# Optimization experiments

Measured on AMD Instinct MI355X. Metric: run time of the kernel, lower is better.

Reference implementation:

```python
import jax, jax.numpy as jnp
import numpy as np

B, S, DMAX, NMEL, DM, K = 8, 100, 12, 80, 128, 9
T = S * DMAX  # 1200 max mel frames
EPS = 1e-5  # BatchNorm eps (eval mode, running_mean=0, running_var=1)


def setup_inputs() -> dict:
    key = jax.random.key(0)
    ks = jax.random.split(key, 16)
    durations = jax.random.randint(ks[0], (B, S), 4, DMAX + 1).astype(jnp.int32)
    mel_len = jnp.sum(durations, axis=1).astype(jnp.int32)
    src_len = jnp.full((B,), S, dtype=jnp.int32)
    mel = jax.random.normal(ks[1], (B, T, NMEL), dtype=jnp.float32)
    # conv stack params (xavier-ish uniform)
    s1 = float(np.sqrt(6.0 / (1 * K + DM * K)))
    w1 = jax.random.uniform(ks[2], (DM, 1, 1, K), minval=-s1, maxval=s1, dtype=jnp.float32)
    g1 = 1.0 + 0.1 * jax.random.normal(ks[3], (DM,), dtype=jnp.float32)
    be1 = 0.1 * jax.random.normal(ks[4], (DM,), dtype=jnp.float32)
    s2 = float(np.sqrt(6.0 / (DM * K + 1 * K)))
    w2 = jax.random.uniform(ks[5], (1, DM, 1, K), minval=-s2, maxval=s2, dtype=jnp.float32)
    g2 = 1.0 + 0.1 * jax.random.normal(ks[6], (1,), dtype=jnp.float32)
    be2 = 0.1 * jax.random.normal(ks[7], (1,), dtype=jnp.float32)
    # BiGRU params (pytorch layout: gates [r|z|n] stacked -> 3*H rows)
    sh = float(1.0 / np.sqrt(DM))
    u = lambda k, shape: jax.random.uniform(k, shape, minval=-sh, maxval=sh, dtype=jnp.float32)
    w_ih_f = u(ks[8], (3 * DM, NMEL)); w_hh_f = u(ks[9], (3 * DM, DM))
    b_ih_f = u(ks[10], (3 * DM,));    b_hh_f = u(ks[11], (3 * DM,))
    w_ih_b = u(ks[12], (3 * DM, NMEL)); w_hh_b = u(ks[13], (3 * DM, DM))
    b_ih_b = u(ks[14], (3 * DM,));    b_hh_b = u(ks[15], (3 * DM,))
    return {"mel": mel, "durations": durations, "mel_len": mel_len, "src_len": src_len,
            "w1": w1, "g1": g1, "be1": be1, "w2": w2, "g2": g2, "be2": be2,
            "w_ih_f": w_ih_f, "w_hh_f": w_hh_f, "b_ih_f": b_ih_f, "b_hh_f": b_hh_f,
            "w_ih_b": w_ih_b, "w_hh_b": w_hh_b, "b_ih_b": b_ih_b, "b_hh_b": b_hh_b}


def _bn_eval(x, g, b):
    # eval-mode BatchNorm2d with running_mean=0, running_var=1; x [B,C,T,M]
    scale = g / jnp.sqrt(1.0 + EPS)
    return x * scale[None, :, None, None] + b[None, :, None, None]


def _gru_scan(xs_seq, reset_seq, w_hh, b_hh):
    # xs_seq [T,B,3H] precomputed input projections; reset_seq [T,B] 1.0 -> reset h to 0
    H = w_hh.shape[1]
    Bn = xs_seq.shape[1]

    def step(h, inp):
        xg, rst = inp
        h = h * (1.0 - rst)[:, None]
        hg = h @ w_hh.T + b_hh
        xr, xz, xn = jnp.split(xg, 3, axis=-1)
        hr, hz, hn = jnp.split(hg, 3, axis=-1)
        r = jax.nn.sigmoid(xr + hr)
        z = jax.nn.sigmoid(xz + hz)
        n = jnp.tanh(xn + r * hn)
        h_new = (1.0 - z) * n + z * h
        return h_new, h_new

    h0 = jnp.zeros((Bn, H), xs_seq.dtype)
    _, hs = jax.lax.scan(step, h0, (xs_seq, reset_seq))
    return hs  # [T,B,H]


def reference(mel, durations, mel_len, src_len, w1, g1, be1, w2, g2, be2,
              w_ih_f, w_hh_f, b_ih_f, b_hh_f, w_ih_b, w_hh_b, b_ih_b, b_hh_b):
    pad = (K - 1) // 2
    # conv stack: kernel (1,K) mixes only the mel-channel axis -> apply to full mel once
    x = mel[:, None, :, :]  # [B,1,T,M]
    x = jax.lax.conv_general_dilated(x, w1, (1, 1), [(0, 0), (pad, pad)])
    x = jax.nn.relu(_bn_eval(x, g1, be1))
    x = jax.lax.conv_general_dilated(x, w2, (1, 1), [(0, 0), (pad, pad)])
    x = jax.nn.relu(_bn_eval(x, g2, be2))
    x = x[:, 0]  # [B,T,M]

    # segment boundaries from durations (all phones valid here, durations > 0)
    cum = jnp.cumsum(durations, axis=1)      # [B,S]
    starts = cum - durations                 # segment start frame per phone
    ends = cum - 1                           # segment end frame per phone
    bidx = jnp.arange(B)[:, None]
    start_mask = jnp.zeros((B, T), x.dtype).at[bidx, starts].set(1.0)
    end_mask = jnp.zeros((B, T), x.dtype).at[bidx, ends].set(1.0)

    # forward direction: reset h at segment starts, read h at segment ends
    xf = jnp.einsum('btm,gm->tbg', x, w_ih_f) + b_ih_f
    Hf = _gru_scan(xf, start_mask.T, w_hh_f, b_hh_f)           # [T,B,H]
    # backward direction: scan reversed time, reset at original segment ends
    xb = jnp.einsum('btm,gm->tbg', x, w_ih_b) + b_ih_b
    Hb = _gru_scan(xb[::-1], end_mask.T[::-1], w_hh_b, b_hh_b)[::-1]  # [T,B,H], orig time

    hf = jnp.take_along_axis(jnp.transpose(Hf, (1, 0, 2)), ends[..., None], axis=1)    # [B,S,H]
    hb = jnp.take_along_axis(jnp.transpose(Hb, (1, 0, 2)), starts[..., None], axis=1)  # [B,S,H]
    out = jnp.concatenate([hf, hb], axis=-1)  # [B,S,2H]
    valid = (jnp.arange(S)[None, :] < src_len[:, None])[..., None]
    return jnp.where(valid, out, 0.0)
```

## Files before the change

### kernel.cpp

```cpp
#include <hip/hip_runtime.h>
#include <math.h>

#define BB   8
#define SS   100
#define TT   1200
#define NM   80
#define DMC  128
#define KK   9
#define G3   384
#define NROW (BB*TT)

typedef __attribute__((ext_vector_type(8))) short short8;
typedef __attribute__((ext_vector_type(4))) float f32x4;
typedef __attribute__((ext_vector_type(2))) float f32x2;

__device__ __forceinline__ float sigmoid_(float v) { return 1.f / (1.f + __expf(-v)); }
__device__ __forceinline__ float tanh_(float v) {
    float a = fabsf(v);
    float e = __expf(-2.f * a);
    float t = (1.f - e) / (1.f + e);
    return copysignf(t, v);
}
__device__ __forceinline__ unsigned short f2bf(float f) {
    unsigned int u = __float_as_uint(f);
    unsigned int r = (u + 0x7fffu + ((u >> 16) & 1u)) >> 16;
    return (unsigned short)r;
}
__device__ __forceinline__ f32x2 pk_fma(f32x2 a, f32x2 b, f32x2 c) {
    f32x2 d;
    asm("v_pk_fma_f32 %0, %1, %2, %3" : "=v"(d) : "v"(a), "v"(b), "v"(c));
    return d;
}
__device__ __forceinline__ f32x2 pk_add(f32x2 a, f32x2 b) {
    f32x2 d;
    asm("v_pk_add_f32 %0, %1, %2" : "=v"(d) : "v"(a), "v"(b));
    return d;
}

__global__ __launch_bounds__(256) void k_convprep(
    const float* __restrict__ mel, const int* __restrict__ mel_len,
    const float* __restrict__ w1, const float* __restrict__ g1, const float* __restrict__ be1,
    const float* __restrict__ w2, const float* __restrict__ g2, const float* __restrict__ be2,
    float* __restrict__ xout,
    const float* __restrict__ whf, const float* __restrict__ whb,
    const float* __restrict__ wif, const float* __restrict__ wib,
    const float* __restrict__ bf, const float* __restrict__ bbv,
    const int* __restrict__ dur,
    unsigned short* __restrict__ wph, unsigned short* __restrict__ wpl,
    unsigned short* __restrict__ wih_h, unsigned short* __restrict__ wih_l,
    float* __restrict__ biasc, int* __restrict__ starts) {
    int bx = blockIdx.x;
    int b  = blockIdx.y;
    int tid = threadIdx.x;

    if (bx >= 600) {
        int pid = (bx - 600) * 8 + b;
        if (pid < 87) {
            int u = pid * 256 + tid;
            if (u < 12288) {
                int idx = u;
                int lane = idx & 63;
                int k32  = (idx >> 6) & 3;
                int tau  = (idx >> 8) % 24;
                int dir  = idx / (24 * 4 * 64);
                const float* w = dir ? whb : whf;
                int gg = tau * 16 + (lane & 15);
                int kbase = k32 * 32 + (lane >> 4) * 8;
#pragma unroll
                for (int j = 0; j < 8; j++) {
                    float v = w[gg * DMC + kbase + j];
                    unsigned short hi = f2bf(v);
                    float hif = __uint_as_float(((unsigned)hi) << 16);
                    unsigned short lo = f2bf(v - hif);
                    wph[idx * 8 + j] = hi;
                    wpl[idx * 8 + j] = lo;
                }
            } else if (u < 21504) {
                int idx = u - 12288;
                int lane = idx & 63;
                int ks   = (idx >> 6) % 3;
                int tau  = idx / (3 * 64);
                int gate = tau * 16 + (lane & 15);
                int kb   = ks * 32 + (lane >> 4) * 8;
                const float* w = (gate < G3) ? (wif + gate * NM) : (wib + (gate - G3) * NM);
#pragma unroll
                for (int j = 0; j < 8; j++) {
                    int k = kb + j;
                    float v = (k < NM) ? w[k] : 0.f;
                    unsigned short hi = f2bf(v);
                    float hif = __uint_as_float(((unsigned)hi) << 16);
                    unsigned short lo = f2bf(v - hif);
                    wih_h[idx * 8 + j] = hi;
                    wih_l[idx * 8 + j] = lo;
                }
            } else {
                int v = u - 21504;
                biasc[v] = (v < G3) ? bf[v] : bbv[v - G3];
            }
        } else {
            int batch = tid >> 5, l = tid & 31;
            int run = 0;
#pragma unroll
            for (int c = 0; c < 4; c++) {
                int s = c * 32 + l;
                int v = (s < SS) ? dur[batch * SS + s] : 0;
                int xv = v;
#pragma unroll
                for (int off = 1; off < 32; off <<= 1) {
                    int t = __shfl_up(xv, off, 32);
                    if (l >= off) xv += t;
                }
                if (s < SS) starts[batch * SS + s] = run + xv - v;
                run += __shfl(xv, 31, 32);
            }
        }
        return;
    }

    int t0 = bx * 2;
    int ml = mel_len[b];
    if (t0 >= ml) return;

    __shared__ __align__(16) f32x2 mp2[96];
    __shared__ __align__(16) f32x2 part2[8][82];

    int mq = tid >> 6, g = tid & 63;
    int ms = 20 * mq;
    const float inv_sqrt = 0.9999950000374997f;

    if (tid < 192) {
        int rr = tid / 96, i = tid - rr * 96;
        float v = 0.f;
        if (i >= 8 && i < 88) v = mel[(b * TT + t0 + rr) * NM + i - 8];
        ((float*)mp2)[i * 2 + rr] = v;
    }
    __syncthreads();

    f32x2 c[20];
#pragma unroll
    for (int m = 0; m < 20; m++) c[m] = (f32x2){0.f, 0.f};

#pragma unroll 1
    for (int dd = 0; dd < 2; dd++) {
        int d = g + 64 * dd;
        float sc = g1[d] * inv_sqrt;
        f32x2 w1p[KK], w2p[KK];
#pragma unroll
        for (int k = 0; k < KK; k++) {
            float a  = w1[d * KK + k] * sc;
            float bq = w2[d * KK + k];
            w1p[k] = (f32x2){a, a};
            w2p[k] = (f32x2){bq, bq};
        }
        float sb = be1[d];
        f32x2 sbp = (f32x2){sb, sb};

        f32x2 mw[12];
        {
            const float4* p4 = (const float4*)(mp2 + ms);
#pragma unroll
            for (int q = 0; q < 6; q++) {
                float4 v = p4[q];
                mw[2 * q]     = (f32x2){v.x, v.y};
                mw[2 * q + 1] = (f32x2){v.z, v.w};
            }
        }
#pragma unroll
        for (int ch = 0; ch < 7; ch++) {
            bool live = true;
            if (ch == 0) live = (mq != 0);
            if (ch == 6) live = (mq != 3);
            if (live) {
                f32x2 yv4[4];
#pragma unroll
                for (int jj = 0; jj < 4; jj++) {
                    f32x2 yv = sbp;
#pragma unroll
                    for (int k = 0; k < KK; k++) yv = pk_fma(w1p[k], mw[jj + k], yv);
                    yv[0] = fmaxf(yv[0], 0.f);
                    yv[1] = fmaxf(yv[1], 0.f);
                    yv4[jj] = yv;
                }
#pragma unroll
                for (int jj = 0; jj < 4; jj++) {
                    int off = ch * 4 + jj;
#pragma unroll
                    for (int k = 0; k < KK; k++) {
                        int mo = off - k;
                        if (mo >= 0 && mo < 20) c[mo] = pk_fma(w2p[k], yv4[jj], c[mo]);
                    }
                }
            }
            if (ch < 6) {
#pragma unroll
                for (int q = 0; q < 8; q++) mw[q] = mw[q + 4];
                const float4* p4 = (const float4*)(mp2 + ms + ch * 4 + 12);
                float4 a0 = p4[0], a1 = p4[1];
                mw[8]  = (f32x2){a0.x, a0.y};
                mw[9]  = (f32x2){a0.z, a0.w};
                mw[10] = (f32x2){a1.x, a1.y};
                mw[11] = (f32x2){a1.z, a1.w};
            }
        }
    }

#pragma unroll
    for (int m = 0; m < 20; m++) {
        f32x2 o;
        o[0] = __shfl_xor(c[m][0], 1);
        o[1] = __shfl_xor(c[m][1], 1);
        c[m] = pk_add(c[m], o);
        o[0] = __shfl_xor(c[m][0], 2);
        o[1] = __shfl_xor(c[m][1], 2);
        c[m] = pk_add(c[m], o);
        o[0] = __shfl_xor(c[m][0], 4);
        o[1] = __shfl_xor(c[m][1], 4);
        c[m] = pk_add(c[m], o);
    }
    if ((g & 7) == 0) {
        int p = g >> 3;
#pragma unroll
        for (int m = 0; m < 20; m++) part2[p][ms + m] = c[m];
    }
    __syncthreads();

    if (tid < 160) {
        int rr = (tid >= 80) ? 1 : 0;
        int m  = tid - 80 * rr;
        int t  = t0 + rr;
        if (t < ml) {
            float s = 0.f;
#pragma unroll
            for (int p = 0; p < 8; p++) s += part2[p][m][rr];
            float v = fmaxf(0.f, fmaf(s, g2[0] * inv_sqrt, be2[0]));
            xout[(b * TT + t) * NM + m] = v;
        }
    }
}

__global__ __launch_bounds__(512, 2) void k_gru(
    const float* __restrict__ x,
    const unsigned short* __restrict__ wph, const unsigned short* __restrict__ wpl,
    const unsigned short* __restrict__ wih_h, const unsigned short* __restrict__ wih_l,
    const float* __restrict__ biasc,
    const int* __restrict__ dur_all, const int* __restrict__ starts,
    const int* __restrict__ src_len,
    const float* __restrict__ bhf, const float* __restrict__ bhb,
    float* __restrict__ out) {
    int sblk = blockIdx.x;
    int b    = blockIdx.y;
    int dir  = blockIdx.z;
    int s0 = sblk * 16;

    __shared__ __align__(16) short8 xbh[12][192];
    __shared__ __align__(16) short8 xbl[12][192];
    __shared__ __align__(16) unsigned short hbh[2][2048];
    __shared__ __align__(16) unsigned short hbl[2][2048];
    __shared__ int sdur[16], sstart[16];

    int tid  = threadIdx.x;
    int wave = tid >> 6, lane = tid & 63;
    int quad = lane >> 4, seg = lane & 15;

    if (tid < 16) {
        int ss = s0 + tid;
        sdur[tid]   = (ss < SS) ? dur_all[b * SS + ss] : 0;
        sstart[tid] = (ss < SS) ? starts[b * SS + ss]  : 0;
    }
    for (int i = tid; i < 2048; i += 512) { hbh[0][i] = 0; hbl[0][i] = 0; }

    short8 Ah[3][4], Al[3][4];
    const short8* wph8 = (const short8*)wph;
    const short8* wpl8 = (const short8*)wpl;
#pragma unroll
    for (int tt = 0; tt < 3; tt++)
#pragma unroll
        for (int k32 = 0; k32 < 4; k32++) {
            int idx = ((dir * 24 + wave + 8 * tt) * 4 + k32) * 64 + lane;
            Ah[tt][k32] = wph8[idx];
            Al[tt][k32] = wpl8[idx];
        }
    short8 Gh[3][3], Gl[3][3];
    const short8* wih_h8 = (const short8*)wih_h;
    const short8* wih_l8 = (const short8*)wih_l;
#pragma unroll
    for (int tt = 0; tt < 3; tt++)
#pragma unroll
        for (int ks = 0; ks < 3; ks++) {
            int idx = ((dir * 24 + wave + 8 * tt) * 3 + ks) * 64 + lane;
            Gh[tt][ks] = wih_h8[idx];
            Gl[tt][ks] = wih_l8[idx];
        }

    int s = s0 + seg;
    int sd = (s < SS) ? dur_all[b * SS + s] : 0;
    int slb = src_len[b];
    const float* bih = biasc + dir * G3;
    const float* bhh = dir ? bhb : bhf;
    int j0 = wave * 16 + quad * 4;
    float4 i_r = *(const float4*)&bih[j0];
    float4 i_z = *(const float4*)&bih[DMC + j0];
    float4 bxn = *(const float4*)&bih[2 * DMC + j0];
    float4 h_r = *(const float4*)&bhh[j0];
    float4 h_z = *(const float4*)&bhh[DMC + j0];
    float4 bhn = *(const float4*)&bhh[2 * DMC + j0];
    float4 br = make_float4(i_r.x + h_r.x, i_r.y + h_r.y, i_r.z + h_r.z, i_r.w + h_r.w);
    float4 bz = make_float4(i_z.x + h_z.x, i_z.y + h_z.y, i_z.z + h_z.z, i_z.w + h_z.w);
    float4 h = make_float4(0.f, 0.f, 0.f, 0.f);

    int idx8 = (j0 >> 5) * 64 + ((j0 >> 3) & 3) * 16 + seg;
    int wbase = idx8 * 8 + (j0 & 7);

    __syncthreads();

#pragma unroll
    for (int q = 0; q < 5; q++) {
        int u = tid + q * 512;
        if (u < 12 * 192) {
            int it  = u / 192;
            int rem = u - it * 192;
            int ks = rem >> 6, ln = rem & 63;
            int sg = ln & 15, qq = ln >> 4;
            int kb = ks * 32 + qq * 8;
            short8 hi8 = {0,0,0,0,0,0,0,0}, lo8 = {0,0,0,0,0,0,0,0};
            int d2 = sdur[sg];
            if (kb < NM && it < d2) {
                int t = dir ? (sstart[sg] + d2 - 1 - it) : (sstart[sg] + it);
                const float* xr = x + (size_t)(b * TT + t) * NM + kb;
#pragma unroll
                for (int j = 0; j < 8; j++) {
                    float v = xr[j];
                    unsigned short hi = f2bf(v);
                    hi8[j] = (short)hi;
                    lo8[j] = (short)f2bf(v - __uint_as_float(((unsigned)hi) << 16));
                }
            }
            xbh[it][rem] = hi8;
            xbl[it][rem] = lo8;
        }
    }
    __syncthreads();

    for (int i = 0; i < 12; i++) {
        int p = i & 1;
        bool act = (i < sd);

        f32x4 axr = (f32x4){0.f,0.f,0.f,0.f};
        f32x4 axz = (f32x4){0.f,0.f,0.f,0.f};
        f32x4 axn = (f32x4){0.f,0.f,0.f,0.f};
        f32x4 ahr = (f32x4){0.f,0.f,0.f,0.f};
        f32x4 ahz = (f32x4){0.f,0.f,0.f,0.f};
        f32x4 ahn = (f32x4){0.f,0.f,0.f,0.f};
#pragma unroll
        for (int ks = 0; ks < 3; ks++) {
            short8 Bxh = xbh[i][ks * 64 + lane];
            short8 Bxl = xbl[i][ks * 64 + lane];
            axr = __builtin_amdgcn_mfma_f32_16x16x32_bf16(Gh[0][ks], Bxh, axr, 0, 0, 0);
            axr = __builtin_amdgcn_mfma_f32_16x16x32_bf16(Gh[0][ks], Bxl, axr, 0, 0, 0);
            axr = __builtin_amdgcn_mfma_f32_16x16x32_bf16(Gl[0][ks], Bxh, axr, 0, 0, 0);
            axz = __builtin_amdgcn_mfma_f32_16x16x32_bf16(Gh[1][ks], Bxh, axz, 0, 0, 0);
            axz = __builtin_amdgcn_mfma_f32_16x16x32_bf16(Gh[1][ks], Bxl, axz, 0, 0, 0);
            axz = __builtin_amdgcn_mfma_f32_16x16x32_bf16(Gl[1][ks], Bxh, axz, 0, 0, 0);
            axn = __builtin_amdgcn_mfma_f32_16x16x32_bf16(Gh[2][ks], Bxh, axn, 0, 0, 0);
            axn = __builtin_amdgcn_mfma_f32_16x16x32_bf16(Gh[2][ks], Bxl, axn, 0, 0, 0);
            axn = __builtin_amdgcn_mfma_f32_16x16x32_bf16(Gl[2][ks], Bxh, axn, 0, 0, 0);
        }
#pragma unroll
        for (int k32 = 0; k32 < 4; k32++) {
            short8 Bh = ((const short8*)hbh[p])[k32 * 64 + lane];
            short8 Bl = ((const short8*)hbl[p])[k32 * 64 + lane];
            ahr = __builtin_amdgcn_mfma_f32_16x16x32_bf16(Ah[0][k32], Bh, ahr, 0, 0, 0);
            ahr = __builtin_amdgcn_mfma_f32_16x16x32_bf16(Ah[0][k32], Bl, ahr, 0, 0, 0);
            ahr = __builtin_amdgcn_mfma_f32_16x16x32_bf16(Al[0][k32], Bh, ahr, 0, 0, 0);
            ahz = __builtin_amdgcn_mfma_f32_16x16x32_bf16(Ah[1][k32], Bh, ahz, 0, 0, 0);
            ahz = __builtin_amdgcn_mfma_f32_16x16x32_bf16(Ah[1][k32], Bl, ahz, 0, 0, 0);
            ahz = __builtin_amdgcn_mfma_f32_16x16x32_bf16(Al[1][k32], Bh, ahz, 0, 0, 0);
            ahn = __builtin_amdgcn_mfma_f32_16x16x32_bf16(Ah[2][k32], Bh, ahn, 0, 0, 0);
            ahn = __builtin_amdgcn_mfma_f32_16x16x32_bf16(Ah[2][k32], Bl, ahn, 0, 0, 0);
            ahn = __builtin_amdgcn_mfma_f32_16x16x32_bf16(Al[2][k32], Bh, ahn, 0, 0, 0);
        }

        if (act) {
            float hv[4]  = {h.x, h.y, h.z, h.w};
            float brv[4] = {br.x, br.y, br.z, br.w};
            float bzv[4] = {bz.x, bz.y, bz.z, bz.w};
            float bxv[4] = {bxn.x, bxn.y, bxn.z, bxn.w};
            float bhv[4] = {bhn.x, bhn.y, bhn.z, bhn.w};
#pragma unroll
            for (int cmp = 0; cmp < 4; cmp++) {
                float r = sigmoid_(axr[cmp] + ahr[cmp] + brv[cmp]);
                float z = sigmoid_(axz[cmp] + ahz[cmp] + bzv[cmp]);
                float n = tanh_(axn[cmp] + bxv[cmp] + r * (ahn[cmp] + bhv[cmp]));
                hv[cmp] = (1.f - z) * n + z * hv[cmp];
            }
            h = make_float4(hv[0], hv[1], hv[2], hv[3]);
            if (i == sd - 1) {
                float4 vout = (s < slb) ? h : make_float4(0.f, 0.f, 0.f, 0.f);
                *(float4*)&out[(b * SS + s) * (2 * DMC) + dir * DMC + j0] = vout;
            }
        }

        {
            float hv[4] = {h.x, h.y, h.z, h.w};
            unsigned short hs_[4], ls_[4];
#pragma unroll
            for (int cmp = 0; cmp < 4; cmp++) {
                unsigned short hi = f2bf(hv[cmp]);
                float hif = __uint_as_float(((unsigned)hi) << 16);
                hs_[cmp] = hi;
                ls_[cmp] = f2bf(hv[cmp] - hif);
            }
            *(ushort4*)&hbh[1 - p][wbase] = make_ushort4(hs_[0], hs_[1], hs_[2], hs_[3]);
            *(ushort4*)&hbl[1 - p][wbase] = make_ushort4(ls_[0], ls_[1], ls_[2], ls_[3]);
        }
        __syncthreads();
    }
}

extern "C" void kernel_launch(void* const* d_in, const int* in_sizes, int n_in,
                              void* d_out, int out_size, void* d_ws, size_t ws_size,
                              hipStream_t stream) {
    const float* mel      = (const float*)d_in[0];
    const int*   durations= (const int*)  d_in[1];
    const int*   mel_len  = (const int*)  d_in[2];
    const int*   src_len  = (const int*)  d_in[3];
    const float* w1       = (const float*)d_in[4];
    const float* g1       = (const float*)d_in[5];
    const float* be1      = (const float*)d_in[6];
    const float* w2       = (const float*)d_in[7];
    const float* g2       = (const float*)d_in[8];
    const float* be2      = (const float*)d_in[9];
    const float* w_ih_f   = (const float*)d_in[10];
    const float* w_hh_f   = (const float*)d_in[11];
    const float* b_ih_f   = (const float*)d_in[12];
    const float* b_hh_f   = (const float*)d_in[13];
    const float* w_ih_b   = (const float*)d_in[14];
    const float* w_hh_b   = (const float*)d_in[15];
    const float* b_ih_b   = (const float*)d_in[16];
    const float* b_hh_b   = (const float*)d_in[17];
    float* out = (float*)d_out;

    float* x    = (float*)d_ws;
    unsigned short* wph   = (unsigned short*)(x + NROW * NM);
    unsigned short* wpl   = wph + 2 * 24 * 4 * 64 * 8;
    unsigned short* wih_h = wpl + 2 * 24 * 4 * 64 * 8;
    unsigned short* wih_l = wih_h + 48 * 3 * 64 * 8;
    float* biasc = (float*)(wih_l + 48 * 3 * 64 * 8);
    int*   starts= (int*)(biasc + 768);

    k_convprep<<<dim3(611, BB), 256, 0, stream>>>(
        mel, mel_len, w1, g1, be1, w2, g2, be2, x,
        w_hh_f, w_hh_b, w_ih_f, w_ih_b, b_ih_f, b_ih_b,
        durations, wph, wpl, wih_h, wih_l, biasc, starts);
    k_gru<<<dim3(7, 8, 2), 512, 0, stream>>>(x, wph, wpl, wih_h, wih_l, biasc,
                                             durations, starts, src_len,
                                             b_hh_f, b_hh_b, out);
}
```

Baseline: 154.3 us.

## Process four frame pairs per conv block with double-buffered smem and DPP reductions

Each conv block now handles 8 frames (4 pairs) instead of 2. The mel rows for the next pair are prefetched into a second shared buffer while the current pair is computed, and the final reduce/store of the previous pair overlaps the current one. The grid shrinks from 611 to 161 blocks in x, which cuts per-block launch and setup overhead. The xor-shuffle reduction is replaced with DPP and ds_swizzle moves, which are cheaper than ds_bpermute. The trade-off is less parallelism, since far fewer blocks may leave CUs idle, and the per-pair work is serialised inside each block.

```diff
diff --git a/kernel.cpp b/kernel.cpp
--- a/kernel.cpp
+++ b/kernel.cpp
@@ -35,6 +35,24 @@
     f32x2 d;
     asm("v_pk_add_f32 %0, %1, %2" : "=v"(d) : "v"(a), "v"(b));
     return d;
+}
+__device__ __forceinline__ f32x2 red_x1(f32x2 c) {
+    f32x2 o;
+    o[0] = __int_as_float(__builtin_amdgcn_mov_dpp(__float_as_int(c[0]), 0xB1, 0xF, 0xF, true));
+    o[1] = __int_as_float(__builtin_amdgcn_mov_dpp(__float_as_int(c[1]), 0xB1, 0xF, 0xF, true));
+    return pk_add(c, o);
+}
+__device__ __forceinline__ f32x2 red_x2(f32x2 c) {
+    f32x2 o;
+    o[0] = __int_as_float(__builtin_amdgcn_mov_dpp(__float_as_int(c[0]), 0x4E, 0xF, 0xF, true));
+    o[1] = __int_as_float(__builtin_amdgcn_mov_dpp(__float_as_int(c[1]), 0x4E, 0xF, 0xF, true));
+    return pk_add(c, o);
+}
+__device__ __forceinline__ f32x2 red_x4(f32x2 c) {
+    f32x2 o;
+    o[0] = __int_as_float(__builtin_amdgcn_ds_swizzle(__float_as_int(c[0]), 0x101F));
+    o[1] = __int_as_float(__builtin_amdgcn_ds_swizzle(__float_as_int(c[1]), 0x101F));
+    return pk_add(c, o);
 }
 
 __global__ __launch_bounds__(256) void k_convprep(
@@ -53,8 +71,8 @@
     int b  = blockIdx.y;
     int tid = threadIdx.x;
 
-    if (bx >= 600) {
-        int pid = (bx - 600) * 8 + b;
+    if (bx >= 150) {
+        int pid = (bx - 150) * 8 + b;
         if (pid < 87) {
             int u = pid * 256 + tid;
             if (u < 12288) {
@@ -62,8 +80,8 @@
                 int lane = idx & 63;
                 int k32  = (idx >> 6) & 3;
                 int tau  = (idx >> 8) % 24;
-                int dir  = idx / (24 * 4 * 64);
-                const float* w = dir ? whb : whf;
+                int dirp = idx / (24 * 4 * 64);
+                const float* w = dirp ? whb : whf;
                 int gg = tau * 16 + (lane & 15);
                 int kbase = k32 * 32 + (lane >> 4) * 8;
 #pragma unroll
@@ -117,123 +135,159 @@
         return;
     }
 
-    int t0 = bx * 2;
     int ml = mel_len[b];
-    if (t0 >= ml) return;
-
-    __shared__ __align__(16) f32x2 mp2[96];
-    __shared__ __align__(16) f32x2 part2[8][82];
+    int tbase = bx * 8;
+    if (tbase >= ml) return;
+
+    __shared__ __align__(16) f32x2 mp2[2][96];
+    __shared__ __align__(16) f32x2 part2[2][8][82];
 
     int mq = tid >> 6, g = tid & 63;
     int ms = 20 * mq;
     const float inv_sqrt = 0.9999950000374997f;
-
-    if (tid < 192) {
-        int rr = tid / 96, i = tid - rr * 96;
+    float g2s  = g2[0] * inv_sqrt;
+    float be2s = be2[0];
+
+    bool stthr = (tid < 192);
+    int rr_s = 0, i_s = 0;
+    if (stthr) { rr_s = tid / 96; i_s = tid - rr_s * 96; }
+
+    if (stthr) {
         float v = 0.f;
-        if (i >= 8 && i < 88) v = mel[(b * TT + t0 + rr) * NM + i - 8];
-        ((float*)mp2)[i * 2 + rr] = v;
+        if (i_s >= 8 && i_s < 88) v = mel[(b * TT + tbase + rr_s) * NM + i_s - 8];
+        ((float*)mp2[0])[i_s * 2 + rr_s] = v;
     }
     __syncthreads();
 
-    f32x2 c[20];
-#pragma unroll
-    for (int m = 0; m < 20; m++) c[m] = (f32x2){0.f, 0.f};
-
 #pragma unroll 1
-    for (int dd = 0; dd < 2; dd++) {
-        int d = g + 64 * dd;
-        float sc = g1[d] * inv_sqrt;
-        f32x2 w1p[KK], w2p[KK];
-#pragma unroll
-        for (int k = 0; k < KK; k++) {
-            float a  = w1[d * KK + k] * sc;
-            float bq = w2[d * KK + k];
-            w1p[k] = (f32x2){a, a};
-            w2p[k] = (f32x2){bq, bq};
-        }
-        float sb = be1[d];
-        f32x2 sbp = (f32x2){sb, sb};
-
-        f32x2 mw[12];
-        {
-            const float4* p4 = (const float4*)(mp2 + ms);
-#pragma unroll
-            for (int q = 0; q < 6; q++) {
-                float4 v = p4[q];
-                mw[2 * q]     = (f32x2){v.x, v.y};
-                mw[2 * q + 1] = (f32x2){v.z, v.w};
-            }
-        }
-#pragma unroll
-        for (int ch = 0; ch < 7; ch++) {
-            bool live = true;
-            if (ch == 0) live = (mq != 0);
-            if (ch == 6) live = (mq != 3);
-            if (live) {
-                f32x2 yv4[4];
-#pragma unroll
-                for (int jj = 0; jj < 4; jj++) {
-                    f32x2 yv = sbp;
-#pragma unroll
-                    for (int k = 0; k < KK; k++) yv = pk_fma(w1p[k], mw[jj + k], yv);
-                    yv[0] = fmaxf(yv[0], 0.f);
-                    yv[1] = fmaxf(yv[1], 0.f);
-                    yv4[jj] = yv;
-                }
-#pragma unroll
-                for (int jj = 0; jj < 4; jj++) {
-                    int off = ch * 4 + jj;
-#pragma unroll
-                    for (int k = 0; k < KK; k++) {
-                        int mo = off - k;
-                        if (mo >= 0 && mo < 20) c[mo] = pk_fma(w2p[k], yv4[jj], c[mo]);
+    for (int pp = 0; pp < 4; pp++) {
+        int cur = pp & 1;
+        int t0 = tbase + pp * 2;
+        bool live = (t0 < ml);
+
+        float sv = 0.f;
+        bool willst = stthr && (pp < 3);
+        if (willst && i_s >= 8 && i_s < 88)
+            sv = mel[(b * TT + t0 + 2 + rr_s) * NM + i_s - 8];
+
+        if (live) {
+            f32x2 c[20];
+#pragma unroll
+            for (int m = 0; m < 20; m++) c[m] = (f32x2){0.f, 0.f};
+
+#pragma unroll 1
+            for (int dd = 0; dd < 2; dd++) {
+                int d = g + 64 * dd;
+                float sc = g1[d] * inv_sqrt;
+                f32x2 w1p[KK], w2p[KK];
+#pragma unroll
+                for (int k = 0; k < KK; k++) {
+                    float a  = w1[d * KK + k] * sc;
+                    float bq = w2[d * KK + k];
+                    w1p[k] = (f32x2){a, a};
+                    w2p[k] = (f32x2){bq, bq};
+                }
+                float sb = be1[d];
+                f32x2 sbp = (f32x2){sb, sb};
+
+                f32x2 mw[12];
+                {
+                    const float4* p4 = (const float4*)(mp2[cur] + ms);
+#pragma unroll
+                    for (int q = 0; q < 6; q++) {
+                        float4 v = p4[q];
+                        mw[2 * q]     = (f32x2){v.x, v.y};
+                        mw[2 * q + 1] = (f32x2){v.z, v.w};
                     }
                 }
-            }
-            if (ch < 6) {
-#pragma unroll
-                for (int q = 0; q < 8; q++) mw[q] = mw[q + 4];
-                const float4* p4 = (const float4*)(mp2 + ms + ch * 4 + 12);
-                float4 a0 = p4[0], a1 = p4[1];
-                mw[8]  = (f32x2){a0.x, a0.y};
-                mw[9]  = (f32x2){a0.z, a0.w};
-                mw[10] = (f32x2){a1.x, a1.y};
-                mw[11] = (f32x2){a1.z, a1.w};
-            }
-        }
-    }
-
-#pragma unroll
-    for (int m = 0; m < 20; m++) {
-        f32x2 o;
-        o[0] = __shfl_xor(c[m][0], 1);
-        o[1] = __shfl_xor(c[m][1], 1);
-        c[m] = pk_add(c[m], o);
-        o[0] = __shfl_xor(c[m][0], 2);
-        o[1] = __shfl_xor(c[m][1], 2);
-        c[m] = pk_add(c[m], o);
-        o[0] = __shfl_xor(c[m][0], 4);
-        o[1] = __shfl_xor(c[m][1], 4);
-        c[m] = pk_add(c[m], o);
-    }
-    if ((g & 7) == 0) {
-        int p = g >> 3;
-#pragma unroll
-        for (int m = 0; m < 20; m++) part2[p][ms + m] = c[m];
-    }
-    __syncthreads();
-
-    if (tid < 160) {
-        int rr = (tid >= 80) ? 1 : 0;
-        int m  = tid - 80 * rr;
-        int t  = t0 + rr;
-        if (t < ml) {
-            float s = 0.f;
-#pragma unroll
-            for (int p = 0; p < 8; p++) s += part2[p][m][rr];
-            float v = fmaxf(0.f, fmaf(s, g2[0] * inv_sqrt, be2[0]));
-            xout[(b * TT + t) * NM + m] = v;
+#pragma unroll
+                for (int ch = 0; ch < 7; ch++) {
+                    bool liveg = true;
+                    if (ch == 0) liveg = (mq != 0);
+                    if (ch == 6) liveg = (mq != 3);
+                    if (liveg) {
+                        f32x2 yv4[4];
+#pragma unroll
+                        for (int jj = 0; jj < 4; jj++) {
+                            f32x2 yv = sbp;
+#pragma unroll
+                            for (int k = 0; k < KK; k++) yv = pk_fma(w1p[k], mw[jj + k], yv);
+                            yv[0] = fmaxf(yv[0], 0.f);
+                            yv[1] = fmaxf(yv[1], 0.f);
+                            yv4[jj] = yv;
+                        }
+#pragma unroll
+                        for (int jj = 0; jj < 4; jj++) {
+                            int off = ch * 4 + jj;
+#pragma unroll
+                            for (int k = 0; k < KK; k++) {
+                                int mo = off - k;
+                                if (mo >= 0 && mo < 20) c[mo] = pk_fma(w2p[k], yv4[jj], c[mo]);
+                            }
+                        }
+                    }
+                    if (ch < 6) {
+#pragma unroll
+                        for (int q = 0; q < 8; q++) mw[q] = mw[q + 4];
+                        const float4* p4 = (const float4*)(mp2[cur] + ms + ch * 4 + 12);
+                        float4 a0 = p4[0], a1 = p4[1];
+                        mw[8]  = (f32x2){a0.x, a0.y};
+                        mw[9]  = (f32x2){a0.z, a0.w};
+                        mw[10] = (f32x2){a1.x, a1.y};
+                        mw[11] = (f32x2){a1.z, a1.w};
+                    }
+                }
+            }
+
+#pragma unroll
+            for (int m = 0; m < 20; m++) {
+                c[m] = red_x1(c[m]);
+                c[m] = red_x2(c[m]);
+                c[m] = red_x4(c[m]);
+            }
+            if ((g & 7) == 0) {
+                int p = g >> 3;
+#pragma unroll
+                for (int m = 0; m < 20; m++) part2[cur][p][ms + m] = c[m];
+            }
+        }
+
+        if (pp > 0) {
+            int t0p = tbase + (pp - 1) * 2;
+            if (t0p < ml && tid < 160) {
+                int rr = (tid >= 80) ? 1 : 0;
+                int m  = tid - 80 * rr;
+                int t  = t0p + rr;
+                if (t < ml) {
+                    float s = 0.f;
+#pragma unroll
+                    for (int p = 0; p < 8; p++) s += part2[1 - cur][p][m][rr];
+                    float v = fmaxf(0.f, fmaf(s, g2s, be2s));
+                    xout[(b * TT + t) * NM + m] = v;
+                }
+            }
+        }
+
+        if (willst) {
+            float v = (i_s >= 8 && i_s < 88) ? sv : 0.f;
+            ((float*)mp2[1 - cur])[i_s * 2 + rr_s] = v;
+        }
+        __syncthreads();
+    }
+
+    {
+        int t0p = tbase + 6;
+        if (t0p < ml && tid < 160) {
+            int rr = (tid >= 80) ? 1 : 0;
+            int m  = tid - 80 * rr;
+            int t  = t0p + rr;
+            if (t < ml) {
+                float s = 0.f;
+#pragma unroll
+                for (int p = 0; p < 8; p++) s += part2[1][p][m][rr];
+                float v = fmaxf(0.f, fmaf(s, g2s, be2s));
+                xout[(b * TT + t) * NM + m] = v;
+            }
         }
     }
 }
@@ -448,7 +502,7 @@
     float* biasc = (float*)(wih_l + 48 * 3 * 64 * 8);
     int*   starts= (int*)(biasc + 768);
 
-    k_convprep<<<dim3(611, BB), 256, 0, stream>>>(
+    k_convprep<<<dim3(161, BB), 256, 0, stream>>>(
         mel, mel_len, w1, g1, be1, w2, g2, be2, x,
         w_hh_f, w_hh_b, w_ih_f, w_ih_b, b_ih_f, b_ih_b,
         durations, wph, wpl, wih_h, wih_l, biasc, starts);
```

Result: slower. 164.3 us (+6.5%).
